# Optimization experiments

Measured on AMD Instinct MI355X. Metric: run time of the kernel, lower is better.

## Reference

```python
import jax, jax.numpy as jnp
import numpy as np

TY = 10  # decoder loop uses the global Ty=10 in the original code


def _bi_lstm_dir(X, Wih, Whh, b, n_hidden):
    # X: (m, T, F); returns hidden states (m, T, n_hidden). Gate order: i,f,g,o.
    m = X.shape[0]
    def step(carry, x_t):
        h, c = carry
        g = x_t @ Wih.T + h @ Whh.T + b
        i, f, gg, o = jnp.split(g, 4, axis=-1)
        c = jax.nn.sigmoid(f) * c + jax.nn.sigmoid(i) * jnp.tanh(gg)
        h = jax.nn.sigmoid(o) * jnp.tanh(c)
        return (h, c), h
    h0 = jnp.zeros((m, n_hidden), X.dtype)
    _, hs = jax.lax.scan(step, (h0, h0), jnp.swapaxes(X, 0, 1))
    return jnp.swapaxes(hs, 0, 1)


def setup_inputs() -> dict:
    key = jax.random.key(0)
    ks = jax.random.split(key, 17)
    m, Tx, F = 256, 256, 128
    n_a, n_s, vocab, attn_h = 256, 512, 1024, 10
    def w(k, shape, fan_in):
        return (jax.random.normal(k, shape, jnp.float32) / np.sqrt(fan_in)).astype(jnp.float32)
    return {
        "X": jax.random.normal(ks[0], (m, Tx, F), jnp.float32),
        "Wih_f": w(ks[1], (4 * n_a, F), F),
        "Whh_f": w(ks[2], (4 * n_a, n_a), n_a),
        "b_f": w(ks[3], (4 * n_a,), n_a),
        "Wih_b": w(ks[4], (4 * n_a, F), F),
        "Whh_b": w(ks[5], (4 * n_a, n_a), n_a),
        "b_b": w(ks[6], (4 * n_a,), n_a),
        "W1": w(ks[7], (attn_h, 2 * n_a + n_s), 2 * n_a + n_s),
        "b1": w(ks[8], (attn_h,), attn_h),
        "W2": w(ks[9], (1, attn_h), attn_h),
        "b2": w(ks[10], (1,), attn_h),
        "Wc_ih": w(ks[11], (4 * n_s, n_s), n_s),
        "Wc_hh": w(ks[12], (4 * n_s, n_s), n_s),
        "bc": w(ks[13], (4 * n_s,), n_s),
        "Wfc": w(ks[14], (vocab, n_s), n_s),
        "bfc": w(ks[15], (vocab,), n_s),
    }


def reference(X, Wih_f, Whh_f, b_f, Wih_b, Whh_b, b_b, W1, b1, W2, b2, Wc_ih, Wc_hh, bc, Wfc, bfc):
    m, Tx, _ = X.shape
    n_a = Whh_f.shape[1]
    n_s = Wc_hh.shape[1]
    # bidirectional encoder
    a_f = _bi_lstm_dir(X, Wih_f, Whh_f, b_f, n_a)
    a_b = _bi_lstm_dir(X[:, ::-1], Wih_b, Whh_b, b_b, n_a)[:, ::-1]
    a = jnp.concatenate([a_f, a_b], axis=-1)  # (m, Tx, 2*n_a)
    # decoder: initial h_n = zeros(m, 2, n_a).flatten(1) == zeros(m, n_s) since n_s = 2*n_a
    s = jnp.zeros((m, n_s), X.dtype)
    c = jnp.zeros((m, n_s), X.dtype)
    outs = []
    for _ in range(TY):
        sp = jnp.broadcast_to(s[:, None, :], (m, Tx, n_s))
        concat = jnp.concatenate([a, sp], axis=-1)           # (m, Tx, 2*n_a + n_s)
        e = jnp.tanh(concat @ W1.T + b1)                     # (m, Tx, 10)
        scores = jax.nn.relu(e @ W2.T + b2)                  # (m, Tx, 1)
        alphas = jax.nn.softmax(scores, axis=1)              # softmax over Tx
        context = jnp.sum(alphas * a, axis=1)                # (m, 2*n_a) == (m, n_s)
        g = context @ Wc_ih.T + s @ Wc_hh.T + bc             # LSTMCell
        i, f, gg, o = jnp.split(g, 4, axis=-1)
        c = jax.nn.sigmoid(f) * c + jax.nn.sigmoid(i) * jnp.tanh(gg)
        s = jax.nn.sigmoid(o) * jnp.tanh(c)
        outs.append(s @ Wfc.T + bfc)                         # (m, vocab)
    return jnp.stack(outs, axis=1)                           # (m, Ty, vocab)
```

## Files before the change

kernel.cpp:

```cpp
#include <hip/hip_runtime.h>
#include <hip/hip_bf16.h>
#include <hip/hip_cooperative_groups.h>

namespace cg = cooperative_groups;

#define TXN 256
#define NA 256
#define NF 128
#define NS 512
#define TYN 10
#define VOCAB 1024

#define A_STR 392
#define W_STR 392
#define WL_OFF (64 * W_STR)
#define AH_OFF (2 * 64 * W_STR)
#define AL_OFF (AH_OFF + 32 * A_STR)
#define PRE_OFF_US (AL_OFF + 32 * A_STR)
#define ENC_LDS_BYTES (150528 + 32 * 68 * 4 + 64 * 4)

#define D_STR 264
#define D_WH 0
#define D_WL (64 * D_STR)
#define D_AH (2 * 64 * D_STR)
#define D_AL (D_AH + 32 * D_STR)
#define D_PRE_US (D_AL + 32 * D_STR)
#define DEC_LDS_BYTES (101376 + 32 * 68 * 4 + 64 * 4)

typedef __attribute__((ext_vector_type(8))) short bf16x8;
typedef __attribute__((ext_vector_type(4))) float f32x4;

__device__ __forceinline__ float fsigmoid(float x) { return 1.f / (1.f + __expf(-x)); }
__device__ __forceinline__ float ftanh(float x)    { return 1.f - 2.f / (1.f + __expf(2.f * x)); }

__device__ __forceinline__ void split_bf16(float v, unsigned short& hi, unsigned short& lo) {
    __hip_bfloat16 h = __float2bfloat16(v);
    float rem = v - __bfloat162float(h);
    __hip_bfloat16 l = __float2bfloat16(rem);
    hi = *reinterpret_cast<unsigned short*>(&h);
    lo = *reinterpret_cast<unsigned short*>(&l);
}

__global__ __launch_bounds__(256, 1) void encoder_kernel(
    const float* __restrict__ X,
    const float* __restrict__ Wih_f, const float* __restrict__ Whh_f, const float* __restrict__ b_f,
    const float* __restrict__ Wih_b, const float* __restrict__ Whh_b, const float* __restrict__ b_b,
    float* __restrict__ a, unsigned int* __restrict__ bar)
{
    extern __shared__ unsigned char smem_raw[];
    unsigned short* Wh  = (unsigned short*)smem_raw;
    unsigned short* Wl  = (unsigned short*)smem_raw + WL_OFF;
    unsigned short* Ahh = (unsigned short*)smem_raw + AH_OFF;
    unsigned short* All = (unsigned short*)smem_raw + AL_OFF;
    float* Pre = (float*)(smem_raw + (size_t)PRE_OFF_US * 2);
    float* bsh = Pre + 32 * 68;

    const int tid = threadIdx.x;
    const int dir = blockIdx.x & 1;
    const int bid = blockIdx.x >> 1;
    const int i0 = (bid >> 4) * 32;
    const int j0 = (bid & 15) * 16;
    const int grp = dir * 8 + (bid >> 4);
    const int myjb = bid & 15;
    unsigned int* slots = bar + grp * 16;

    const float* __restrict__ Wih = dir ? Wih_b : Wih_f;
    const float* __restrict__ Whh = dir ? Whh_b : Whh_f;
    const float* __restrict__ bv  = dir ? b_b  : b_f;

    const int jl = tid & 15;
    const int ip = tid >> 4;
    const int iA = ip * 2;

    if (tid < 64) bsh[tid] = bv[(tid >> 4) * NA + j0 + (tid & 15)];
    for (int r = 0; r < 64; ++r) {
        int row = (r >> 4) * NA + j0 + (r & 15);
        unsigned short hi, lo;
        split_bf16(Whh[(size_t)row * NA + tid], hi, lo);
        Wh[r * W_STR + tid] = hi;
        Wl[r * W_STR + tid] = lo;
        if (tid < NF) {
            split_bf16(Wih[(size_t)row * NF + tid], hi, lo);
            Wh[r * W_STR + 256 + tid] = hi;
            Wl[r * W_STR + 256 + tid] = lo;
        }
    }

    #pragma unroll 4
    for (int r = 0; r < 32; ++r) {
        Ahh[r * A_STR + tid] = 0;
        All[r * A_STR + tid] = 0;
    }
    {
        const int t0 = dir ? (TXN - 1) : 0;
        const int kx = tid & 127;
        const int rbase = tid >> 7;
        #pragma unroll 4
        for (int rr = 0; rr < 16; ++rr) {
            int r = rr * 2 + rbase;
            float v = X[((size_t)(i0 + r) * TXN + t0) * NF + kx];
            unsigned short hi, lo;
            split_bf16(v, hi, lo);
            Ahh[r * A_STR + 256 + kx] = hi;
            All[r * A_STR + 256 + kx] = lo;
        }
    }

    float c0 = 0.f, c1 = 0.f;

    const int lane = tid & 63;
    const int wv   = tid >> 6;
    const int rt   = wv >> 1;
    const int g0   = (wv & 1) * 2;
    const int ln   = lane & 15;
    const int quad = lane >> 4;
    const unsigned short* pAh = Ahh + (rt * 16 + ln) * A_STR + quad * 8;
    const unsigned short* pAl = All + (rt * 16 + ln) * A_STR + quad * 8;
    const unsigned short* pW0h = Wh + (g0 * 16 + ln) * W_STR + quad * 8;
    const unsigned short* pW0l = Wl + (g0 * 16 + ln) * W_STR + quad * 8;
    const unsigned short* pW1h = pW0h + 16 * W_STR;
    const unsigned short* pW1l = pW0l + 16 * W_STR;

    for (int step = 0; step < TXN; ++step) {
        const int t = dir ? (TXN - 1 - step) : step;

        if (step != 0) {
            const int tprev = dir ? (t + 1) : (t - 1);
            const int jb = tid >> 4;
            while (__hip_atomic_load(&slots[jb], __ATOMIC_RELAXED,
                                     __HIP_MEMORY_SCOPE_AGENT) < (unsigned)step) {}
            float hv[32];
            #pragma unroll
            for (int r = 0; r < 32; ++r) {
                hv[r] = __hip_atomic_load(
                    &a[(((size_t)(i0 + r) * TXN + tprev) << 9) + dir * NA + tid],
                    __ATOMIC_RELAXED, __HIP_MEMORY_SCOPE_AGENT);
            }
            #pragma unroll
            for (int r = 0; r < 32; ++r) {
                unsigned short hi, lo;
                split_bf16(hv[r], hi, lo);
                Ahh[r * A_STR + tid] = hi;
                All[r * A_STR + tid] = lo;
            }
        }
        __syncthreads();

        f32x4 a0e = {0.f,0.f,0.f,0.f}, a0o = {0.f,0.f,0.f,0.f};
        f32x4 a1e = {0.f,0.f,0.f,0.f}, a1o = {0.f,0.f,0.f,0.f};
        #pragma unroll
        for (int kp = 0; kp < 6; ++kp) {
            {
                const int kc = kp * 2;
                bf16x8 fah = *(const bf16x8*)(pAh + kc * 32);
                bf16x8 fal = *(const bf16x8*)(pAl + kc * 32);
                bf16x8 w0h = *(const bf16x8*)(pW0h + kc * 32);
                bf16x8 w0l = *(const bf16x8*)(pW0l + kc * 32);
                bf16x8 w1h = *(const bf16x8*)(pW1h + kc * 32);
                bf16x8 w1l = *(const bf16x8*)(pW1l + kc * 32);
                a0e = __builtin_amdgcn_mfma_f32_16x16x32_bf16(fal, w0h, a0e, 0, 0, 0);
                a0e = __builtin_amdgcn_mfma_f32_16x16x32_bf16(fah, w0l, a0e, 0, 0, 0);
                a0e = __builtin_amdgcn_mfma_f32_16x16x32_bf16(fah, w0h, a0e, 0, 0, 0);
                a1e = __builtin_amdgcn_mfma_f32_16x16x32_bf16(fal, w1h, a1e, 0, 0, 0);
                a1e = __builtin_amdgcn_mfma_f32_16x16x32_bf16(fah, w1l, a1e, 0, 0, 0);
                a1e = __builtin_amdgcn_mfma_f32_16x16x32_bf16(fah, w1h, a1e, 0, 0, 0);
            }
            {
                const int kc = kp * 2 + 1;
                bf16x8 fah = *(const bf16x8*)(pAh + kc * 32);
                bf16x8 fal = *(const bf16x8*)(pAl + kc * 32);
                bf16x8 w0h = *(const bf16x8*)(pW0h + kc * 32);
                bf16x8 w0l = *(const bf16x8*)(pW0l + kc * 32);
                bf16x8 w1h = *(const bf16x8*)(pW1h + kc * 32);
                bf16x8 w1l = *(const bf16x8*)(pW1l + kc * 32);
                a0o = __builtin_amdgcn_mfma_f32_16x16x32_bf16(fal, w0h, a0o, 0, 0, 0);
                a0o = __builtin_amdgcn_mfma_f32_16x16x32_bf16(fah, w0l, a0o, 0, 0, 0);
                a0o = __builtin_amdgcn_mfma_f32_16x16x32_bf16(fah, w0h, a0o, 0, 0, 0);
                a1o = __builtin_amdgcn_mfma_f32_16x16x32_bf16(fal, w1h, a1o, 0, 0, 0);
                a1o = __builtin_amdgcn_mfma_f32_16x16x32_bf16(fah, w1l, a1o, 0, 0, 0);
                a1o = __builtin_amdgcn_mfma_f32_16x16x32_bf16(fah, w1h, a1o, 0, 0, 0);
            }
        }
        #pragma unroll
        for (int reg = 0; reg < 4; ++reg) {
            int prow = rt * 16 + quad * 4 + reg;
            Pre[prow * 68 + g0 * 16 + ln]       = a0e[reg] + a0o[reg];
            Pre[prow * 68 + (g0 + 1) * 16 + ln] = a1e[reg] + a1o[reg];
        }
        __syncthreads();

        float h0, h1;
        {
            float gi = fsigmoid(Pre[iA * 68 +      jl] + bsh[jl]);
            float gf = fsigmoid(Pre[iA * 68 + 16 + jl] + bsh[16 + jl]);
            float gg = ftanh  (Pre[iA * 68 + 32 + jl] + bsh[32 + jl]);
            float go = fsigmoid(Pre[iA * 68 + 48 + jl] + bsh[48 + jl]);
            c0 = gf * c0 + gi * gg;
            h0 = go * ftanh(c0);
        }
        {
            float gi = fsigmoid(Pre[(iA + 1) * 68 +      jl] + bsh[jl]);
            float gf = fsigmoid(Pre[(iA + 1) * 68 + 16 + jl] + bsh[16 + jl]);
            float gg = ftanh  (Pre[(iA + 1) * 68 + 32 + jl] + bsh[32 + jl]);
            float go = fsigmoid(Pre[(iA + 1) * 68 + 48 + jl] + bsh[48 + jl]);
            c1 = gf * c1 + gi * gg;
            h1 = go * ftanh(c1);
        }
        __hip_atomic_store(
            &a[(((size_t)(i0 + iA)     * TXN + t) << 9) + dir * NA + j0 + jl],
            h0, __ATOMIC_RELAXED, __HIP_MEMORY_SCOPE_AGENT);
        __hip_atomic_store(
            &a[(((size_t)(i0 + iA + 1) * TXN + t) << 9) + dir * NA + j0 + jl],
            h1, __ATOMIC_RELAXED, __HIP_MEMORY_SCOPE_AGENT);

        if (step != TXN - 1) {
            __syncthreads();
            if (tid == 0) {
                __hip_atomic_store(&slots[myjb], (unsigned)(step + 1),
                                   __ATOMIC_RELAXED, __HIP_MEMORY_SCOPE_AGENT);
            }
            {
                const int tn = dir ? (t - 1) : (t + 1);
                const int kx = tid & 127;
                const int rbase = tid >> 7;
                #pragma unroll 4
                for (int rr = 0; rr < 16; ++rr) {
                    int r = rr * 2 + rbase;
                    float v = X[((size_t)(i0 + r) * TXN + tn) * NF + kx];
                    unsigned short hi, lo;
                    split_bf16(v, hi, lo);
                    Ahh[r * A_STR + 256 + kx] = hi;
                    All[r * A_STR + 256 + kx] = lo;
                }
            }
        }
    }
}

__global__ __launch_bounds__(256) void wsplit_cat(
    const float* __restrict__ Wc_ih, const float* __restrict__ Wc_hh,
    unsigned short* __restrict__ Wh, unsigned short* __restrict__ Wl)
{
    int idx = blockIdx.x * 256 + threadIdx.x;
    int r = idx >> 10, k = idx & 1023;
    float v = (k < 512) ? Wc_ih[(size_t)r * 512 + k] : Wc_hh[(size_t)r * 512 + (k - 512)];
    unsigned short hi, lo;
    split_bf16(v, hi, lo);
    Wh[idx] = hi; Wl[idx] = lo;
}

__global__ __launch_bounds__(256) void wsplit_fc(
    const float* __restrict__ Wfc,
    unsigned short* __restrict__ Wh, unsigned short* __restrict__ Wl)
{
    int idx = blockIdx.x * 256 + threadIdx.x;
    unsigned short hi, lo;
    split_bf16(Wfc[idx], hi, lo);
    Wh[idx] = hi; Wl[idx] = lo;
}

__global__ __launch_bounds__(256, 1) void gates_kernel(
    const float* __restrict__ xcat,
    const unsigned short* __restrict__ Wch,
    const unsigned short* __restrict__ Wcl,
    const float* __restrict__ bc,
    float* __restrict__ c_buf,
    float* __restrict__ s_buf,
    float* __restrict__ xc_out)
{
    extern __shared__ unsigned char smem_raw[];
    unsigned short* Wh = (unsigned short*)smem_raw + D_WH;
    unsigned short* Wl = (unsigned short*)smem_raw + D_WL;
    unsigned short* Ah = (unsigned short*)smem_raw + D_AH;
    unsigned short* Al = (unsigned short*)smem_raw + D_AL;
    float* Pre = (float*)(smem_raw + (size_t)D_PRE_US * 2);
    float* bsh = Pre + 32 * 68;

    const int tid = threadIdx.x;
    const int i0 = blockIdx.x * 32;
    const int j0 = blockIdx.y * 16;

    if (tid < 64) bsh[tid] = bc[(tid >> 4) * 512 + j0 + (tid & 15)];

    const int lane = tid & 63;
    const int wv   = tid >> 6;
    const int rt   = wv >> 1;
    const int g0   = (wv & 1) * 2;
    const int ln   = lane & 15;
    const int quad = lane >> 4;
    const unsigned short* pAh = Ah + (rt * 16 + ln) * D_STR + quad * 8;
    const unsigned short* pAl = Al + (rt * 16 + ln) * D_STR + quad * 8;
    const unsigned short* pW0h = Wh + (g0 * 16 + ln) * D_STR + quad * 8;
    const unsigned short* pW0l = Wl + (g0 * 16 + ln) * D_STR + quad * 8;
    const unsigned short* pW1h = pW0h + 16 * D_STR;
    const unsigned short* pW1l = pW0l + 16 * D_STR;

    const int rW = tid >> 2;
    const int qW = (tid & 3) * 64;
    const int rowg = (rW >> 4) * 512 + j0 + (rW & 15);

    f32x4 a0 = {0.f,0.f,0.f,0.f}, a1 = {0.f,0.f,0.f,0.f};

    for (int ch = 0; ch < 4; ++ch) {
        const int kc0 = ch * 256;
        __syncthreads();
        #pragma unroll 8
        for (int r = 0; r < 32; ++r) {
            float v = xcat[(size_t)(i0 + r) * 1024 + kc0 + tid];
            unsigned short hi, lo;
            split_bf16(v, hi, lo);
            Ah[r * D_STR + tid] = hi;
            Al[r * D_STR + tid] = lo;
        }
        {
            const size_t base = (size_t)rowg * 1024 + kc0 + qW;
            #pragma unroll
            for (int i = 0; i < 8; ++i) {
                *(bf16x8*)&Wh[rW * D_STR + qW + i * 8] = *(const bf16x8*)&Wch[base + i * 8];
                *(bf16x8*)&Wl[rW * D_STR + qW + i * 8] = *(const bf16x8*)&Wcl[base + i * 8];
            }
        }
        __syncthreads();
        #pragma unroll
        for (int kc = 0; kc < 8; ++kc) {
            bf16x8 fah = *(const bf16x8*)(pAh + kc * 32);
            bf16x8 fal = *(const bf16x8*)(pAl + kc * 32);
            bf16x8 w0h = *(const bf16x8*)(pW0h + kc * 32);
            bf16x8 w0l = *(const bf16x8*)(pW0l + kc * 32);
            bf16x8 w1h = *(const bf16x8*)(pW1h + kc * 32);
            bf16x8 w1l = *(const bf16x8*)(pW1l + kc * 32);
            a0 = __builtin_amdgcn_mfma_f32_16x16x32_bf16(fal, w0h, a0, 0, 0, 0);
            a0 = __builtin_amdgcn_mfma_f32_16x16x32_bf16(fah, w0l, a0, 0, 0, 0);
            a0 = __builtin_amdgcn_mfma_f32_16x16x32_bf16(fah, w0h, a0, 0, 0, 0);
            a1 = __builtin_amdgcn_mfma_f32_16x16x32_bf16(fal, w1h, a1, 0, 0, 0);
            a1 = __builtin_amdgcn_mfma_f32_16x16x32_bf16(fah, w1l, a1, 0, 0, 0);
            a1 = __builtin_amdgcn_mfma_f32_16x16x32_bf16(fah, w1h, a1, 0, 0, 0);
        }
    }
    #pragma unroll
    for (int reg = 0; reg < 4; ++reg) {
        int prow = rt * 16 + quad * 4 + reg;
        Pre[prow * 68 + g0 * 16 + ln]       = a0[reg];
        Pre[prow * 68 + (g0 + 1) * 16 + ln] = a1[reg];
    }
    __syncthreads();

    const int jl = tid & 15;
    const int iA = (tid >> 4) * 2;
    #pragma unroll
    for (int rr = 0; rr < 2; ++rr) {
        int r = iA + rr;
        float gi = fsigmoid(Pre[r * 68 +      jl] + bsh[jl]);
        float gf = fsigmoid(Pre[r * 68 + 16 + jl] + bsh[16 + jl]);
        float gg = ftanh  (Pre[r * 68 + 32 + jl] + bsh[32 + jl]);
        float go = fsigmoid(Pre[r * 68 + 48 + jl] + bsh[48 + jl]);
        size_t ci = (size_t)(i0 + r) * 512 + j0 + jl;
        float cn = gf * c_buf[ci] + gi * gg;
        c_buf[ci] = cn;
        float h = go * ftanh(cn);
        s_buf[ci] = h;
        xc_out[(size_t)(i0 + r) * 1024 + 512 + j0 + jl] = h;
    }
}

__global__ __launch_bounds__(256, 1) void logits_kernel(
    const float* __restrict__ s_buf,
    const unsigned short* __restrict__ Wfh,
    const unsigned short* __restrict__ Wfl,
    const float* __restrict__ bfc,
    float* __restrict__ out, int ty)
{
    extern __shared__ unsigned char smem_raw[];
    unsigned short* Wh = (unsigned short*)smem_raw + D_WH;
    unsigned short* Wl = (unsigned short*)smem_raw + D_WL;
    unsigned short* Ah = (unsigned short*)smem_raw + D_AH;
    unsigned short* Al = (unsigned short*)smem_raw + D_AL;

    const int tid = threadIdx.x;
    const int i0 = blockIdx.x * 32;
    const int v0 = blockIdx.y * 64;

    const int lane = tid & 63;
    const int wv   = tid >> 6;
    const int rt   = wv >> 1;
    const int ct   = wv & 1;
    const int ln   = lane & 15;
    const int quad = lane >> 4;
    const unsigned short* pAh = Ah + (rt * 16 + ln) * D_STR + quad * 8;
    const unsigned short* pAl = Al + (rt * 16 + ln) * D_STR + quad * 8;
    const unsigned short* pW0h = Wh + (ct * 32 + ln) * D_STR + quad * 8;
    const unsigned short* pW0l = Wl + (ct * 32 + ln) * D_STR + quad * 8;
    const unsigned short* pW1h = pW0h + 16 * D_STR;
    const unsigned short* pW1l = pW0l + 16 * D_STR;

    const int rW = tid >> 2;
    const int qW = (tid & 3) * 64;

    f32x4 a0 = {0.f,0.f,0.f,0.f}, a1 = {0.f,0.f,0.f,0.f};

    for (int ch = 0; ch < 2; ++ch) {
        const int kc0 = ch * 256;
        __syncthreads();
        #pragma unroll 8
        for (int r = 0; r < 32; ++r) {
            float v = s_buf[(size_t)(i0 + r) * 512 + kc0 + tid];
            unsigned short hi, lo;
            split_bf16(v, hi, lo);
            Ah[r * D_STR + tid] = hi;
            Al[r * D_STR + tid] = lo;
        }
        {
            const size_t base = (size_t)(v0 + rW) * 512 + kc0 + qW;
            #pragma unroll
            for (int i = 0; i < 8; ++i) {
                *(bf16x8*)&Wh[rW * D_STR + qW + i * 8] = *(const bf16x8*)&Wfh[base + i * 8];
                *(bf16x8*)&Wl[rW * D_STR + qW + i * 8] = *(const bf16x8*)&Wfl[base + i * 8];
            }
        }
        __syncthreads();
        #pragma unroll
        for (int kc = 0; kc < 8; ++kc) {
            bf16x8 fah = *(const bf16x8*)(pAh + kc * 32);
            bf16x8 fal = *(const bf16x8*)(pAl + kc * 32);
            bf16x8 w0h = *(const bf16x8*)(pW0h + kc * 32);
            bf16x8 w0l = *(const bf16x8*)(pW0l + kc * 32);
            bf16x8 w1h = *(const bf16x8*)(pW1h + kc * 32);
            bf16x8 w1l = *(const bf16x8*)(pW1l + kc * 32);
            a0 = __builtin_amdgcn_mfma_f32_16x16x32_bf16(fal, w0h, a0, 0, 0, 0);
            a0 = __builtin_amdgcn_mfma_f32_16x16x32_bf16(fah, w0l, a0, 0, 0, 0);
            a0 = __builtin_amdgcn_mfma_f32_16x16x32_bf16(fah, w0h, a0, 0, 0, 0);
            a1 = __builtin_amdgcn_mfma_f32_16x16x32_bf16(fal, w1h, a1, 0, 0, 0);
            a1 = __builtin_amdgcn_mfma_f32_16x16x32_bf16(fah, w1l, a1, 0, 0, 0);
            a1 = __builtin_amdgcn_mfma_f32_16x16x32_bf16(fah, w1h, a1, 0, 0, 0);
        }
    }
    #pragma unroll
    for (int reg = 0; reg < 4; ++reg) {
        int row = i0 + rt * 16 + quad * 4 + reg;
        int col0 = v0 + ct * 32 + ln;
        out[(size_t)row * (TYN * VOCAB) + ty * VOCAB + col0]      = a0[reg] + bfc[col0];
        out[(size_t)row * (TYN * VOCAB) + ty * VOCAB + col0 + 16] = a1[reg] + bfc[col0 + 16];
    }
}

__global__ __launch_bounds__(256) void attn_prep(
    const float* __restrict__ a, const float* __restrict__ W1,
    const float* __restrict__ b1, float* __restrict__ aW1)
{
    __shared__ float Wsh[10][516];
    __shared__ float red[64][10][4];
    const int tid = threadIdx.x;
    for (int idx = tid; idx < 10 * 512; idx += 256) {
        int o = idx >> 9, k = idx & 511;
        Wsh[o][k] = W1[o * 1024 + k];
    }
    __syncthreads();
    const int r = tid >> 2, kq = tid & 3;
    const float* ar = a + ((size_t)blockIdx.x * 64 + r) * 512 + kq * 128;
    float acc[10] = {};
    for (int k = 0; k < 128; k += 4) {
        float4 v = *(const float4*)&ar[k];
        #pragma unroll
        for (int o = 0; o < 10; ++o) {
            float4 w = *(const float4*)&Wsh[o][kq * 128 + k];
            acc[o] += v.x * w.x + v.y * w.y + v.z * w.z + v.w * w.w;
        }
    }
    #pragma unroll
    for (int o = 0; o < 10; ++o) red[r][o][kq] = acc[o];
    __syncthreads();
    for (int idx = tid; idx < 640; idx += 256) {
        int rr = idx / 10, o = idx % 10;
        float s = red[rr][o][0] + red[rr][o][1] + red[rr][o][2] + red[rr][o][3] + b1[o];
        aW1[((size_t)blockIdx.x * 64 + rr) * 10 + o] = s;
    }
}

__global__ __launch_bounds__(256) void attn_kernel(
    const float* __restrict__ aW1,
    const float* __restrict__ s_buf,
    const float* __restrict__ W1,
    const float* __restrict__ W2,
    const float* __restrict__ b2,
    const float* __restrict__ a,
    float* __restrict__ xcat)
{
    __shared__ float sh_s[10];
    __shared__ float sh_w2[10];
    __shared__ float sred[160];
    __shared__ float red[256];
    __shared__ float al[256];
    __shared__ float4 ctxred[256];
    const int i = blockIdx.x;
    const int tid = threadIdx.x;

    if (tid < 160) {
        int o = tid >> 4, part = tid & 15;
        const float* srow = s_buf + (size_t)i * 512;
        const float* wrow = W1 + o * 1024 + 512;
        float p = 0.f;
        for (int k = part; k < 512; k += 16) p += srow[k] * wrow[k];
        sred[tid] = p;
    }
    __syncthreads();
    if (tid < 10) {
        float v = 0.f;
        #pragma unroll
        for (int p = 0; p < 16; ++p) v += sred[tid * 16 + p];
        sh_s[tid] = v;
        sh_w2[tid] = W2[tid];
    }
    __syncthreads();

    float sum = b2[0];
    const float* ar = aW1 + ((size_t)i * TXN + tid) * 10;
    #pragma unroll
    for (int h = 0; h < 10; ++h) {
        float e = ftanh(ar[h] + sh_s[h]);
        sum += e * sh_w2[h];
    }
    float sc = fmaxf(sum, 0.f);

    red[tid] = sc;
    __syncthreads();
    for (int s = 128; s > 0; s >>= 1) {
        if (tid < s) red[tid] = fmaxf(red[tid], red[tid + s]);
        __syncthreads();
    }
    float mx = red[0];
    __syncthreads();
    float p = __expf(sc - mx);
    red[tid] = p;
    __syncthreads();
    for (int s = 128; s > 0; s >>= 1) {
        if (tid < s) red[tid] += red[tid + s];
        __syncthreads();
    }
    float inv = 1.f / red[0];
    al[tid] = p * inv;
    __syncthreads();

    const int half = tid >> 7;
    const int q    = tid & 127;
    const float* abase = a + (size_t)i * TXN * NS + q * 4;
    float4 acc = make_float4(0.f, 0.f, 0.f, 0.f);
    #pragma unroll 8
    for (int t = half; t < TXN; t += 2) {
        float w = al[t];
        float4 v = *(const float4*)&abase[(size_t)t * NS];
        acc.x += w * v.x; acc.y += w * v.y; acc.z += w * v.z; acc.w += w * v.w;
    }
    ctxred[tid] = acc;
    __syncthreads();
    if (tid < 128) {
        float4 e = ctxred[tid];
        float4 o = ctxred[tid + 128];
        float4 r4 = make_float4(e.x + o.x, e.y + o.y, e.z + o.z, e.w + o.w);
        *(float4*)&xcat[(size_t)i * 1024 + tid * 4] = r4;
    }
}

extern "C" void kernel_launch(void* const* d_in, const int* in_sizes, int n_in,
                              void* d_out, int out_size, void* d_ws, size_t ws_size,
                              hipStream_t stream)
{
    const float* X     = (const float*)d_in[0];
    const float* Wih_f = (const float*)d_in[1];
    const float* Whh_f = (const float*)d_in[2];
    const float* b_f   = (const float*)d_in[3];
    const float* Wih_b = (const float*)d_in[4];
    const float* Whh_b = (const float*)d_in[5];
    const float* b_b   = (const float*)d_in[6];
    const float* W1    = (const float*)d_in[7];
    const float* b1    = (const float*)d_in[8];
    const float* W2    = (const float*)d_in[9];
    const float* b2    = (const float*)d_in[10];
    const float* Wc_ih = (const float*)d_in[11];
    const float* Wc_hh = (const float*)d_in[12];
    const float* bc    = (const float*)d_in[13];
    const float* Wfc   = (const float*)d_in[14];
    const float* bfc   = (const float*)d_in[15];
    float* out = (float*)d_out;
    float* ws  = (float*)d_ws;

    float* c_buf = ws;
    float* s_buf = ws + 131072;
    float* xcat  = ws + 262144;
    float* a     = ws + 524288;
    float* aW1   = ws + 34078720;
    unsigned short* Wch = (unsigned short*)(ws + 34734080);
    unsigned short* Wcl = (unsigned short*)(ws + 35782656);
    unsigned short* Wfh = (unsigned short*)(ws + 36831232);
    unsigned short* Wfl = (unsigned short*)(ws + 37093376);
    unsigned int* bar = (unsigned int*)(ws + 37358080);

    static int attrs_set = 0;
    if (!attrs_set) {
        hipFuncSetAttribute(reinterpret_cast<const void*>(encoder_kernel),
                            hipFuncAttributeMaxDynamicSharedMemorySize, ENC_LDS_BYTES);
        hipFuncSetAttribute(reinterpret_cast<const void*>(gates_kernel),
                            hipFuncAttributeMaxDynamicSharedMemorySize, DEC_LDS_BYTES);
        hipFuncSetAttribute(reinterpret_cast<const void*>(logits_kernel),
                            hipFuncAttributeMaxDynamicSharedMemorySize, DEC_LDS_BYTES);
        attrs_set = 1;
    }

    hipMemsetAsync(c_buf, 0, (size_t)524288 * sizeof(float), stream);
    hipMemsetAsync(bar, 0, 16 * 16 * sizeof(unsigned int), stream);

    wsplit_cat<<<8192, 256, 0, stream>>>(Wc_ih, Wc_hh, Wch, Wcl);
    wsplit_fc<<<2048, 256, 0, stream>>>(Wfc, Wfh, Wfl);

    {
        void* args[] = { (void*)&X, (void*)&Wih_f, (void*)&Whh_f, (void*)&b_f,
                         (void*)&Wih_b, (void*)&Whh_b, (void*)&b_b, (void*)&a, (void*)&bar };
        hipLaunchCooperativeKernel(reinterpret_cast<void*>(encoder_kernel),
                                   dim3(256), dim3(256), args, ENC_LDS_BYTES, stream);
    }

    attn_prep<<<1024, 256, 0, stream>>>(a, W1, b1, aW1);

    for (int ty = 0; ty < TYN; ++ty) {
        attn_kernel<<<256, 256, 0, stream>>>(aW1, s_buf, W1, W2, b2, a, xcat);
        gates_kernel<<<dim3(8, 32), 256, DEC_LDS_BYTES, stream>>>(
            xcat, Wch, Wcl, bc, c_buf, s_buf, xcat);
        logits_kernel<<<dim3(8, 16), 256, DEC_LDS_BYTES, stream>>>(
            s_buf, Wfh, Wfl, bfc, out, ty);
    }
}
```

Baseline: 2.194 ms.

## Fuse decoder attention, gates and logits into one persistent cooperative kernel

The 30 per-step decoder launches (attention, LSTM gates, logits for each of 10 output steps) are replaced by a single persistent cooperative kernel of 256 blocks. The blocks coordinate through per-tile flag slots in global memory, with agent-scope atomic loads and stores. The cell state now stays in registers, and the hidden state is double-buffered across two buffers. This removes launch overhead and the round trips through global memory between steps. In exchange it adds spin-wait synchronisation across blocks and a dependency on all 256 blocks being co-resident.

```diff
diff --git a/kernel.cpp b/kernel.cpp
--- a/kernel.cpp
+++ b/kernel.cpp
@@ -39,6 +39,19 @@
     __hip_bfloat16 l = __float2bfloat16(rem);
     hi = *reinterpret_cast<unsigned short*>(&h);
     lo = *reinterpret_cast<unsigned short*>(&l);
+}
+
+__device__ __forceinline__ float agent_ld(const float* p) {
+    return __hip_atomic_load(p, __ATOMIC_RELAXED, __HIP_MEMORY_SCOPE_AGENT);
+}
+__device__ __forceinline__ void agent_st(float* p, float v) {
+    __hip_atomic_store(p, v, __ATOMIC_RELAXED, __HIP_MEMORY_SCOPE_AGENT);
+}
+__device__ __forceinline__ unsigned flag_ld(const unsigned* p) {
+    return __hip_atomic_load(p, __ATOMIC_RELAXED, __HIP_MEMORY_SCOPE_AGENT);
+}
+__device__ __forceinline__ void flag_st(unsigned* p, unsigned v) {
+    __hip_atomic_store(p, v, __ATOMIC_RELAXED, __HIP_MEMORY_SCOPE_AGENT);
 }
 
 __global__ __launch_bounds__(256, 1) void encoder_kernel(
@@ -127,14 +140,11 @@
         if (step != 0) {
             const int tprev = dir ? (t + 1) : (t - 1);
             const int jb = tid >> 4;
-            while (__hip_atomic_load(&slots[jb], __ATOMIC_RELAXED,
-                                     __HIP_MEMORY_SCOPE_AGENT) < (unsigned)step) {}
+            while (flag_ld(&slots[jb]) < (unsigned)step) {}
             float hv[32];
             #pragma unroll
             for (int r = 0; r < 32; ++r) {
-                hv[r] = __hip_atomic_load(
-                    &a[(((size_t)(i0 + r) * TXN + tprev) << 9) + dir * NA + tid],
-                    __ATOMIC_RELAXED, __HIP_MEMORY_SCOPE_AGENT);
+                hv[r] = agent_ld(&a[(((size_t)(i0 + r) * TXN + tprev) << 9) + dir * NA + tid]);
             }
             #pragma unroll
             for (int r = 0; r < 32; ++r) {
@@ -206,19 +216,12 @@
             c1 = gf * c1 + gi * gg;
             h1 = go * ftanh(c1);
         }
-        __hip_atomic_store(
-            &a[(((size_t)(i0 + iA)     * TXN + t) << 9) + dir * NA + j0 + jl],
-            h0, __ATOMIC_RELAXED, __HIP_MEMORY_SCOPE_AGENT);
-        __hip_atomic_store(
-            &a[(((size_t)(i0 + iA + 1) * TXN + t) << 9) + dir * NA + j0 + jl],
-            h1, __ATOMIC_RELAXED, __HIP_MEMORY_SCOPE_AGENT);
+        agent_st(&a[(((size_t)(i0 + iA)     * TXN + t) << 9) + dir * NA + j0 + jl], h0);
+        agent_st(&a[(((size_t)(i0 + iA + 1) * TXN + t) << 9) + dir * NA + j0 + jl], h1);
 
         if (step != TXN - 1) {
             __syncthreads();
-            if (tid == 0) {
-                __hip_atomic_store(&slots[myjb], (unsigned)(step + 1),
-                                   __ATOMIC_RELAXED, __HIP_MEMORY_SCOPE_AGENT);
-            }
+            if (tid == 0) flag_st(&slots[myjb], (unsigned)(step + 1));
             {
                 const int tn = dir ? (t - 1) : (t + 1);
                 const int kx = tid & 127;
@@ -259,190 +262,6 @@
     Wh[idx] = hi; Wl[idx] = lo;
 }
 
-__global__ __launch_bounds__(256, 1) void gates_kernel(
-    const float* __restrict__ xcat,
-    const unsigned short* __restrict__ Wch,
-    const unsigned short* __restrict__ Wcl,
-    const float* __restrict__ bc,
-    float* __restrict__ c_buf,
-    float* __restrict__ s_buf,
-    float* __restrict__ xc_out)
-{
-    extern __shared__ unsigned char smem_raw[];
-    unsigned short* Wh = (unsigned short*)smem_raw + D_WH;
-    unsigned short* Wl = (unsigned short*)smem_raw + D_WL;
-    unsigned short* Ah = (unsigned short*)smem_raw + D_AH;
-    unsigned short* Al = (unsigned short*)smem_raw + D_AL;
-    float* Pre = (float*)(smem_raw + (size_t)D_PRE_US * 2);
-    float* bsh = Pre + 32 * 68;
-
-    const int tid = threadIdx.x;
-    const int i0 = blockIdx.x * 32;
-    const int j0 = blockIdx.y * 16;
-
-    if (tid < 64) bsh[tid] = bc[(tid >> 4) * 512 + j0 + (tid & 15)];
-
-    const int lane = tid & 63;
-    const int wv   = tid >> 6;
-    const int rt   = wv >> 1;
-    const int g0   = (wv & 1) * 2;
-    const int ln   = lane & 15;
-    const int quad = lane >> 4;
-    const unsigned short* pAh = Ah + (rt * 16 + ln) * D_STR + quad * 8;
-    const unsigned short* pAl = Al + (rt * 16 + ln) * D_STR + quad * 8;
-    const unsigned short* pW0h = Wh + (g0 * 16 + ln) * D_STR + quad * 8;
-    const unsigned short* pW0l = Wl + (g0 * 16 + ln) * D_STR + quad * 8;
-    const unsigned short* pW1h = pW0h + 16 * D_STR;
-    const unsigned short* pW1l = pW0l + 16 * D_STR;
-
-    const int rW = tid >> 2;
-    const int qW = (tid & 3) * 64;
-    const int rowg = (rW >> 4) * 512 + j0 + (rW & 15);
-
-    f32x4 a0 = {0.f,0.f,0.f,0.f}, a1 = {0.f,0.f,0.f,0.f};
-
-    for (int ch = 0; ch < 4; ++ch) {
-        const int kc0 = ch * 256;
-        __syncthreads();
-        #pragma unroll 8
-        for (int r = 0; r < 32; ++r) {
-            float v = xcat[(size_t)(i0 + r) * 1024 + kc0 + tid];
-            unsigned short hi, lo;
-            split_bf16(v, hi, lo);
-            Ah[r * D_STR + tid] = hi;
-            Al[r * D_STR + tid] = lo;
-        }
-        {
-            const size_t base = (size_t)rowg * 1024 + kc0 + qW;
-            #pragma unroll
-            for (int i = 0; i < 8; ++i) {
-                *(bf16x8*)&Wh[rW * D_STR + qW + i * 8] = *(const bf16x8*)&Wch[base + i * 8];
-                *(bf16x8*)&Wl[rW * D_STR + qW + i * 8] = *(const bf16x8*)&Wcl[base + i * 8];
-            }
-        }
-        __syncthreads();
-        #pragma unroll
-        for (int kc = 0; kc < 8; ++kc) {
-            bf16x8 fah = *(const bf16x8*)(pAh + kc * 32);
-            bf16x8 fal = *(const bf16x8*)(pAl + kc * 32);
-            bf16x8 w0h = *(const bf16x8*)(pW0h + kc * 32);
-            bf16x8 w0l = *(const bf16x8*)(pW0l + kc * 32);
-            bf16x8 w1h = *(const bf16x8*)(pW1h + kc * 32);
-            bf16x8 w1l = *(const bf16x8*)(pW1l + kc * 32);
-            a0 = __builtin_amdgcn_mfma_f32_16x16x32_bf16(fal, w0h, a0, 0, 0, 0);
-            a0 = __builtin_amdgcn_mfma_f32_16x16x32_bf16(fah, w0l, a0, 0, 0, 0);
-            a0 = __builtin_amdgcn_mfma_f32_16x16x32_bf16(fah, w0h, a0, 0, 0, 0);
-            a1 = __builtin_amdgcn_mfma_f32_16x16x32_bf16(fal, w1h, a1, 0, 0, 0);
-            a1 = __builtin_amdgcn_mfma_f32_16x16x32_bf16(fah, w1l, a1, 0, 0, 0);
-            a1 = __builtin_amdgcn_mfma_f32_16x16x32_bf16(fah, w1h, a1, 0, 0, 0);
-        }
-    }
-    #pragma unroll
-    for (int reg = 0; reg < 4; ++reg) {
-        int prow = rt * 16 + quad * 4 + reg;
-        Pre[prow * 68 + g0 * 16 + ln]       = a0[reg];
-        Pre[prow * 68 + (g0 + 1) * 16 + ln] = a1[reg];
-    }
-    __syncthreads();
-
-    const int jl = tid & 15;
-    const int iA = (tid >> 4) * 2;
-    #pragma unroll
-    for (int rr = 0; rr < 2; ++rr) {
-        int r = iA + rr;
-        float gi = fsigmoid(Pre[r * 68 +      jl] + bsh[jl]);
-        float gf = fsigmoid(Pre[r * 68 + 16 + jl] + bsh[16 + jl]);
-        float gg = ftanh  (Pre[r * 68 + 32 + jl] + bsh[32 + jl]);
-        float go = fsigmoid(Pre[r * 68 + 48 + jl] + bsh[48 + jl]);
-        size_t ci = (size_t)(i0 + r) * 512 + j0 + jl;
-        float cn = gf * c_buf[ci] + gi * gg;
-        c_buf[ci] = cn;
-        float h = go * ftanh(cn);
-        s_buf[ci] = h;
-        xc_out[(size_t)(i0 + r) * 1024 + 512 + j0 + jl] = h;
-    }
-}
-
-__global__ __launch_bounds__(256, 1) void logits_kernel(
-    const float* __restrict__ s_buf,
-    const unsigned short* __restrict__ Wfh,
-    const unsigned short* __restrict__ Wfl,
-    const float* __restrict__ bfc,
-    float* __restrict__ out, int ty)
-{
-    extern __shared__ unsigned char smem_raw[];
-    unsigned short* Wh = (unsigned short*)smem_raw + D_WH;
-    unsigned short* Wl = (unsigned short*)smem_raw + D_WL;
-    unsigned short* Ah = (unsigned short*)smem_raw + D_AH;
-    unsigned short* Al = (unsigned short*)smem_raw + D_AL;
-
-    const int tid = threadIdx.x;
-    const int i0 = blockIdx.x * 32;
-    const int v0 = blockIdx.y * 64;
-
-    const int lane = tid & 63;
-    const int wv   = tid >> 6;
-    const int rt   = wv >> 1;
-    const int ct   = wv & 1;
-    const int ln   = lane & 15;
-    const int quad = lane >> 4;
-    const unsigned short* pAh = Ah + (rt * 16 + ln) * D_STR + quad * 8;
-    const unsigned short* pAl = Al + (rt * 16 + ln) * D_STR + quad * 8;
-    const unsigned short* pW0h = Wh + (ct * 32 + ln) * D_STR + quad * 8;
-    const unsigned short* pW0l = Wl + (ct * 32 + ln) * D_STR + quad * 8;
-    const unsigned short* pW1h = pW0h + 16 * D_STR;
-    const unsigned short* pW1l = pW0l + 16 * D_STR;
-
-    const int rW = tid >> 2;
-    const int qW = (tid & 3) * 64;
-
-    f32x4 a0 = {0.f,0.f,0.f,0.f}, a1 = {0.f,0.f,0.f,0.f};
-
-    for (int ch = 0; ch < 2; ++ch) {
-        const int kc0 = ch * 256;
-        __syncthreads();
-        #pragma unroll 8
-        for (int r = 0; r < 32; ++r) {
-            float v = s_buf[(size_t)(i0 + r) * 512 + kc0 + tid];
-            unsigned short hi, lo;
-            split_bf16(v, hi, lo);
-            Ah[r * D_STR + tid] = hi;
-            Al[r * D_STR + tid] = lo;
-        }
-        {
-            const size_t base = (size_t)(v0 + rW) * 512 + kc0 + qW;
-            #pragma unroll
-            for (int i = 0; i < 8; ++i) {
-                *(bf16x8*)&Wh[rW * D_STR + qW + i * 8] = *(const bf16x8*)&Wfh[base + i * 8];
-                *(bf16x8*)&Wl[rW * D_STR + qW + i * 8] = *(const bf16x8*)&Wfl[base + i * 8];
-            }
-        }
-        __syncthreads();
-        #pragma unroll
-        for (int kc = 0; kc < 8; ++kc) {
-            bf16x8 fah = *(const bf16x8*)(pAh + kc * 32);
-            bf16x8 fal = *(const bf16x8*)(pAl + kc * 32);
-            bf16x8 w0h = *(const bf16x8*)(pW0h + kc * 32);
-            bf16x8 w0l = *(const bf16x8*)(pW0l + kc * 32);
-            bf16x8 w1h = *(const bf16x8*)(pW1h + kc * 32);
-            bf16x8 w1l = *(const bf16x8*)(pW1l + kc * 32);
-            a0 = __builtin_amdgcn_mfma_f32_16x16x32_bf16(fal, w0h, a0, 0, 0, 0);
-            a0 = __builtin_amdgcn_mfma_f32_16x16x32_bf16(fah, w0l, a0, 0, 0, 0);
-            a0 = __builtin_amdgcn_mfma_f32_16x16x32_bf16(fah, w0h, a0, 0, 0, 0);
-            a1 = __builtin_amdgcn_mfma_f32_16x16x32_bf16(fal, w1h, a1, 0, 0, 0);
-            a1 = __builtin_amdgcn_mfma_f32_16x16x32_bf16(fah, w1l, a1, 0, 0, 0);
-            a1 = __builtin_amdgcn_mfma_f32_16x16x32_bf16(fah, w1h, a1, 0, 0, 0);
-        }
-    }
-    #pragma unroll
-    for (int reg = 0; reg < 4; ++reg) {
-        int row = i0 + rt * 16 + quad * 4 + reg;
-        int col0 = v0 + ct * 32 + ln;
-        out[(size_t)row * (TYN * VOCAB) + ty * VOCAB + col0]      = a0[reg] + bfc[col0];
-        out[(size_t)row * (TYN * VOCAB) + ty * VOCAB + col0 + 16] = a1[reg] + bfc[col0 + 16];
-    }
-}
-
 __global__ __launch_bounds__(256) void attn_prep(
     const float* __restrict__ a, const float* __restrict__ W1,
     const float* __restrict__ b1, float* __restrict__ aW1)
@@ -476,87 +295,284 @@
     }
 }
 
-__global__ __launch_bounds__(256) void attn_kernel(
+__global__ __launch_bounds__(256, 1) void decoder_kernel(
     const float* __restrict__ aW1,
-    const float* __restrict__ s_buf,
+    const float* __restrict__ a,
     const float* __restrict__ W1,
     const float* __restrict__ W2,
     const float* __restrict__ b2,
-    const float* __restrict__ a,
-    float* __restrict__ xcat)
+    const unsigned short* __restrict__ Wch,
+    const unsigned short* __restrict__ Wcl,
+    const float* __restrict__ bc,
+    const unsigned short* __restrict__ Wfh,
+    const unsigned short* __restrict__ Wfl,
+    const float* __restrict__ bfc,
+    float* __restrict__ sbufA,
+    float* __restrict__ sbufB,
+    float* __restrict__ xcat,
+    float* __restrict__ out,
+    unsigned int* __restrict__ slots)
 {
-    __shared__ float sh_s[10];
-    __shared__ float sh_w2[10];
-    __shared__ float sred[160];
-    __shared__ float red[256];
-    __shared__ float al[256];
-    __shared__ float4 ctxred[256];
-    const int i = blockIdx.x;
+    extern __shared__ unsigned char smem_raw[];
+    unsigned short* Wh = (unsigned short*)smem_raw + D_WH;
+    unsigned short* Wl = (unsigned short*)smem_raw + D_WL;
+    unsigned short* Ah = (unsigned short*)smem_raw + D_AH;
+    unsigned short* Al = (unsigned short*)smem_raw + D_AL;
+    float* Pre = (float*)(smem_raw + (size_t)D_PRE_US * 2);
+    float* F     = (float*)smem_raw;
+    float* Aal   = F;
+    float* Ared  = F + 256;
+    float* Asred = F + 512;
+    float* Ash_s = F + 672;
+    float* Ash_w2= F + 682;
+    float4* Actx = (float4*)(F + 704);
+
+    unsigned int* attn_slot  = slots;
+    unsigned int* gates_slot = slots + 256;
+    unsigned int* log_slot   = slots + 512;
+
     const int tid = threadIdx.x;
-
-    if (tid < 160) {
-        int o = tid >> 4, part = tid & 15;
-        const float* srow = s_buf + (size_t)i * 512;
-        const float* wrow = W1 + o * 1024 + 512;
-        float p = 0.f;
-        for (int k = part; k < 512; k += 16) p += srow[k] * wrow[k];
-        sred[tid] = p;
-    }
-    __syncthreads();
-    if (tid < 10) {
-        float v = 0.f;
+    const int b   = blockIdx.x;
+    const int it  = b >> 5;
+    const int jt  = b & 31;
+    const int i0  = it * 32;
+    const int j0  = jt * 16;
+    const int v0  = jt * 32;
+
+    const int lane = tid & 63;
+    const int wv   = tid >> 6;
+    const int rt   = wv >> 1;
+    const int g0   = (wv & 1) * 2;
+    const int ct   = wv & 1;
+    const int ln   = lane & 15;
+    const int quad = lane >> 4;
+    const int jl   = tid & 15;
+    const int iA   = (tid >> 4) * 2;
+
+    const unsigned short* pAh = Ah + (rt * 16 + ln) * D_STR + quad * 8;
+    const unsigned short* pAl = Al + (rt * 16 + ln) * D_STR + quad * 8;
+    const unsigned short* pGW0h = Wh + (g0 * 16 + ln) * D_STR + quad * 8;
+    const unsigned short* pGW0l = Wl + (g0 * 16 + ln) * D_STR + quad * 8;
+    const unsigned short* pGW1h = pGW0h + 16 * D_STR;
+    const unsigned short* pGW1l = pGW0l + 16 * D_STR;
+    const unsigned short* pLWh = Wh + (ct * 16 + ln) * D_STR + quad * 8;
+    const unsigned short* pLWl = Wl + (ct * 16 + ln) * D_STR + quad * 8;
+
+    const float bgi = bc[0 * 512 + j0 + jl];
+    const float bgf = bc[1 * 512 + j0 + jl];
+    const float bgg = bc[2 * 512 + j0 + jl];
+    const float bgo = bc[3 * 512 + j0 + jl];
+
+    float c0 = 0.f, c1 = 0.f;
+
+    for (int ty = 0; ty < TYN; ++ty) {
+        float* sp = (ty & 1) ? sbufB : sbufA;
+        float* sn = (ty & 1) ? sbufA : sbufB;
+
+        if (tid < 32) {
+            while (flag_ld(&gates_slot[it * 32 + tid]) < (unsigned)ty) {}
+        }
+        __syncthreads();
+
+        if (tid < 160) {
+            int o = tid >> 4, part = tid & 15;
+            const float* srow = sp + (size_t)b * 512;
+            const float* wrow = W1 + o * 1024 + 512;
+            float p = 0.f;
+            for (int k = part; k < 512; k += 16) p += agent_ld(&srow[k]) * wrow[k];
+            Asred[tid] = p;
+        }
+        __syncthreads();
+        if (tid < 10) {
+            float v = 0.f;
+            #pragma unroll
+            for (int p = 0; p < 16; ++p) v += Asred[tid * 16 + p];
+            Ash_s[tid] = v;
+            Ash_w2[tid] = W2[tid];
+        }
+        __syncthreads();
+
+        float sum = b2[0];
+        {
+            const float* ar = aW1 + ((size_t)b * TXN + tid) * 10;
+            #pragma unroll
+            for (int h = 0; h < 10; ++h) sum += ftanh(ar[h] + Ash_s[h]) * Ash_w2[h];
+        }
+        float sc = fmaxf(sum, 0.f);
+
+        Ared[tid] = sc;
+        __syncthreads();
+        for (int s = 128; s > 0; s >>= 1) {
+            if (tid < s) Ared[tid] = fmaxf(Ared[tid], Ared[tid + s]);
+            __syncthreads();
+        }
+        float mx = Ared[0];
+        __syncthreads();
+        float p = __expf(sc - mx);
+        Ared[tid] = p;
+        __syncthreads();
+        for (int s = 128; s > 0; s >>= 1) {
+            if (tid < s) Ared[tid] += Ared[tid + s];
+            __syncthreads();
+        }
+        float inv = 1.f / Ared[0];
+        Aal[tid] = p * inv;
+        __syncthreads();
+
+        {
+            const int half = tid >> 7;
+            const int q    = tid & 127;
+            const float* abase = a + (size_t)b * TXN * NS + q * 4;
+            float4 acc = make_float4(0.f, 0.f, 0.f, 0.f);
+            #pragma unroll 8
+            for (int t = half; t < TXN; t += 2) {
+                float w = Aal[t];
+                float4 v = *(const float4*)&abase[(size_t)t * NS];
+                acc.x += w * v.x; acc.y += w * v.y; acc.z += w * v.z; acc.w += w * v.w;
+            }
+            Actx[tid] = acc;
+        }
+        __syncthreads();
+        if (tid < 128) {
+            float4 e = Actx[tid];
+            float4 o = Actx[tid + 128];
+            float* dst = &xcat[(size_t)b * 512 + tid * 4];
+            agent_st(dst + 0, e.x + o.x);
+            agent_st(dst + 1, e.y + o.y);
+            agent_st(dst + 2, e.z + o.z);
+            agent_st(dst + 3, e.w + o.w);
+        }
+        __syncthreads();
+        if (tid == 0) flag_st(&attn_slot[b], (unsigned)(ty + 1));
+
+        if (tid < 32) {
+            while (flag_ld(&attn_slot[i0 + tid]) < (unsigned)(ty + 1)) {}
+        } else if (tid < 64) {
+            while (flag_ld(&gates_slot[it * 32 + (tid - 32)]) < (unsigned)ty) {}
+        } else if (tid < 96) {
+            while (flag_ld(&log_slot[it * 32 + (tid - 64)]) < (unsigned)ty) {}
+        }
+
+        f32x4 ga0 = {0.f,0.f,0.f,0.f}, ga1 = {0.f,0.f,0.f,0.f};
+        {
+            const int rW = tid >> 2;
+            const int qW = (tid & 3) * 64;
+            const int rowg = (rW >> 4) * 512 + j0 + (rW & 15);
+            for (int ch = 0; ch < 4; ++ch) {
+                const int kc0 = ch * 256;
+                __syncthreads();
+                #pragma unroll 8
+                for (int r = 0; r < 32; ++r) {
+                    float v;
+                    if (ch < 2) v = agent_ld(&xcat[(size_t)(i0 + r) * 512 + kc0 + tid]);
+                    else        v = agent_ld(&sp[(size_t)(i0 + r) * 512 + (kc0 - 512) + tid]);
+                    unsigned short hi, lo;
+                    split_bf16(v, hi, lo);
+                    Ah[r * D_STR + tid] = hi;
+                    Al[r * D_STR + tid] = lo;
+                }
+                {
+                    const size_t base = (size_t)rowg * 1024 + kc0 + qW;
+                    #pragma unroll
+                    for (int i = 0; i < 8; ++i) {
+                        *(bf16x8*)&Wh[rW * D_STR + qW + i * 8] = *(const bf16x8*)&Wch[base + i * 8];
+                        *(bf16x8*)&Wl[rW * D_STR + qW + i * 8] = *(const bf16x8*)&Wcl[base + i * 8];
+                    }
+                }
+                __syncthreads();
+                #pragma unroll
+                for (int kc = 0; kc < 8; ++kc) {
+                    bf16x8 fah = *(const bf16x8*)(pAh + kc * 32);
+                    bf16x8 fal = *(const bf16x8*)(pAl + kc * 32);
+                    bf16x8 w0h = *(const bf16x8*)(pGW0h + kc * 32);
+                    bf16x8 w0l = *(const bf16x8*)(pGW0l + kc * 32);
+                    bf16x8 w1h = *(const bf16x8*)(pGW1h + kc * 32);
+                    bf16x8 w1l = *(const bf16x8*)(pGW1l + kc * 32);
+                    ga0 = __builtin_amdgcn_mfma_f32_16x16x32_bf16(fal, w0h, ga0, 0, 0, 0);
+                    ga0 = __builtin_amdgcn_mfma_f32_16x16x32_bf16(fah, w0l, ga0, 0, 0, 0);
+                    ga0 = __builtin_amdgcn_mfma_f32_16x16x32_bf16(fah, w0h, ga0, 0, 0, 0);
+                    ga1 = __builtin_amdgcn_mfma_f32_16x16x32_bf16(fal, w1h, ga1, 0, 0, 0);
+                    ga1 = __builtin_amdgcn_mfma_f32_16x16x32_bf16(fah, w1l, ga1, 0, 0, 0);
+                    ga1 = __builtin_amdgcn_mfma_f32_16x16x32_bf16(fah, w1h, ga1, 0, 0, 0);
+                }
+            }
+        }
+        __syncthreads();
         #pragma unroll
-        for (int p = 0; p < 16; ++p) v += sred[tid * 16 + p];
-        sh_s[tid] = v;
-        sh_w2[tid] = W2[tid];
-    }
-    __syncthreads();
-
-    float sum = b2[0];
-    const float* ar = aW1 + ((size_t)i * TXN + tid) * 10;
-    #pragma unroll
-    for (int h = 0; h < 10; ++h) {
-        float e = ftanh(ar[h] + sh_s[h]);
-        sum += e * sh_w2[h];
-    }
-    float sc = fmaxf(sum, 0.f);
-
-    red[tid] = sc;
-    __syncthreads();
-    for (int s = 128; s > 0; s >>= 1) {
-        if (tid < s) red[tid] = fmaxf(red[tid], red[tid + s]);
-        __syncthreads();
-    }
-    float mx = red[0];
-    __syncthreads();
-    float p = __expf(sc - mx);
-    red[tid] = p;
-    __syncthreads();
-    for (int s = 128; s > 0; s >>= 1) {
-        if (tid < s) red[tid] += red[tid + s];
-        __syncthreads();
-    }
-    float inv = 1.f / red[0];
-    al[tid] = p * inv;
-    __syncthreads();
-
-    const int half = tid >> 7;
-    const int q    = tid & 127;
-    const float* abase = a + (size_t)i * TXN * NS + q * 4;
-    float4 acc = make_float4(0.f, 0.f, 0.f, 0.f);
-    #pragma unroll 8
-    for (int t = half; t < TXN; t += 2) {
-        float w = al[t];
-        float4 v = *(const float4*)&abase[(size_t)t * NS];
-        acc.x += w * v.x; acc.y += w * v.y; acc.z += w * v.z; acc.w += w * v.w;
-    }
-    ctxred[tid] = acc;
-    __syncthreads();
-    if (tid < 128) {
-        float4 e = ctxred[tid];
-        float4 o = ctxred[tid + 128];
-        float4 r4 = make_float4(e.x + o.x, e.y + o.y, e.z + o.z, e.w + o.w);
-        *(float4*)&xcat[(size_t)i * 1024 + tid * 4] = r4;
+        for (int reg = 0; reg < 4; ++reg) {
+            int prow = rt * 16 + quad * 4 + reg;
+            Pre[prow * 68 + g0 * 16 + ln]       = ga0[reg];
+            Pre[prow * 68 + (g0 + 1) * 16 + ln] = ga1[reg];
+        }
+        __syncthreads();
+
+        {
+            float gi = fsigmoid(Pre[iA * 68 +      jl] + bgi);
+            float gf = fsigmoid(Pre[iA * 68 + 16 + jl] + bgf);
+            float gg = ftanh  (Pre[iA * 68 + 32 + jl] + bgg);
+            float go = fsigmoid(Pre[iA * 68 + 48 + jl] + bgo);
+            c0 = gf * c0 + gi * gg;
+            agent_st(&sn[(size_t)(i0 + iA) * 512 + j0 + jl], go * ftanh(c0));
+        }
+        {
+            float gi = fsigmoid(Pre[(iA + 1) * 68 +      jl] + bgi);
+            float gf = fsigmoid(Pre[(iA + 1) * 68 + 16 + jl] + bgf);
+            float gg = ftanh  (Pre[(iA + 1) * 68 + 32 + jl] + bgg);
+            float go = fsigmoid(Pre[(iA + 1) * 68 + 48 + jl] + bgo);
+            c1 = gf * c1 + gi * gg;
+            agent_st(&sn[(size_t)(i0 + iA + 1) * 512 + j0 + jl], go * ftanh(c1));
+        }
+        __syncthreads();
+        if (tid == 0) flag_st(&gates_slot[it * 32 + jt], (unsigned)(ty + 1));
+
+        if (tid < 32) {
+            while (flag_ld(&gates_slot[it * 32 + tid]) < (unsigned)(ty + 1)) {}
+        }
+
+        f32x4 lacc = {0.f,0.f,0.f,0.f};
+        {
+            const int rW = tid >> 3;
+            const int qW = (tid & 7) * 32;
+            for (int ch = 0; ch < 2; ++ch) {
+                const int kc0 = ch * 256;
+                __syncthreads();
+                #pragma unroll 8
+                for (int r = 0; r < 32; ++r) {
+                    float v = agent_ld(&sn[(size_t)(i0 + r) * 512 + kc0 + tid]);
+                    unsigned short hi, lo;
+                    split_bf16(v, hi, lo);
+                    Ah[r * D_STR + tid] = hi;
+                    Al[r * D_STR + tid] = lo;
+                }
+                {
+                    const size_t base = (size_t)(v0 + rW) * 512 + kc0 + qW;
+                    #pragma unroll
+                    for (int i = 0; i < 4; ++i) {
+                        *(bf16x8*)&Wh[rW * D_STR + qW + i * 8] = *(const bf16x8*)&Wfh[base + i * 8];
+                        *(bf16x8*)&Wl[rW * D_STR + qW + i * 8] = *(const bf16x8*)&Wfl[base + i * 8];
+                    }
+                }
+                __syncthreads();
+                #pragma unroll
+                for (int kc = 0; kc < 8; ++kc) {
+                    bf16x8 fah = *(const bf16x8*)(pAh + kc * 32);
+                    bf16x8 fal = *(const bf16x8*)(pAl + kc * 32);
+                    bf16x8 wh  = *(const bf16x8*)(pLWh + kc * 32);
+                    bf16x8 wl  = *(const bf16x8*)(pLWl + kc * 32);
+                    lacc = __builtin_amdgcn_mfma_f32_16x16x32_bf16(fal, wh, lacc, 0, 0, 0);
+                    lacc = __builtin_amdgcn_mfma_f32_16x16x32_bf16(fah, wl, lacc, 0, 0, 0);
+                    lacc = __builtin_amdgcn_mfma_f32_16x16x32_bf16(fah, wh, lacc, 0, 0, 0);
+                }
+            }
+        }
+        #pragma unroll
+        for (int reg = 0; reg < 4; ++reg) {
+            int row = i0 + rt * 16 + quad * 4 + reg;
+            int col = v0 + ct * 16 + ln;
+            out[(size_t)row * (TYN * VOCAB) + ty * VOCAB + col] = lacc[reg] + bfc[col];
+        }
+        __syncthreads();
+        if (tid == 0) flag_st(&log_slot[it * 32 + jt], (unsigned)(ty + 1));
     }
 }
 
@@ -583,8 +599,8 @@
     float* out = (float*)d_out;
     float* ws  = (float*)d_ws;
 
-    float* c_buf = ws;
-    float* s_buf = ws + 131072;
+    float* sbufA = ws;
+    float* sbufB = ws + 131072;
     float* xcat  = ws + 262144;
     float* a     = ws + 524288;
     float* aW1   = ws + 34078720;
@@ -592,21 +608,20 @@
     unsigned short* Wcl = (unsigned short*)(ws + 35782656);
     unsigned short* Wfh = (unsigned short*)(ws + 36831232);
     unsigned short* Wfl = (unsigned short*)(ws + 37093376);
-    unsigned int* bar = (unsigned int*)(ws + 37358080);
+    unsigned int* dslots = (unsigned int*)(ws + 37355520);
+    unsigned int* bar    = (unsigned int*)(ws + 37356288);
 
     static int attrs_set = 0;
     if (!attrs_set) {
         hipFuncSetAttribute(reinterpret_cast<const void*>(encoder_kernel),
                             hipFuncAttributeMaxDynamicSharedMemorySize, ENC_LDS_BYTES);
-        hipFuncSetAttribute(reinterpret_cast<const void*>(gates_kernel),
-                            hipFuncAttributeMaxDynamicSharedMemorySize, DEC_LDS_BYTES);
-        hipFuncSetAttribute(reinterpret_cast<const void*>(logits_kernel),
+        hipFuncSetAttribute(reinterpret_cast<const void*>(decoder_kernel),
                             hipFuncAttributeMaxDynamicSharedMemorySize, DEC_LDS_BYTES);
         attrs_set = 1;
     }
 
-    hipMemsetAsync(c_buf, 0, (size_t)524288 * sizeof(float), stream);
-    hipMemsetAsync(bar, 0, 16 * 16 * sizeof(unsigned int), stream);
+    hipMemsetAsync(sbufA, 0, (size_t)131072 * sizeof(float), stream);
+    hipMemsetAsync(dslots, 0, (768 + 256) * sizeof(unsigned int), stream);
 
     wsplit_cat<<<8192, 256, 0, stream>>>(Wc_ih, Wc_hh, Wch, Wcl);
     wsplit_fc<<<2048, 256, 0, stream>>>(Wfc, Wfh, Wfl);
@@ -620,11 +635,13 @@
 
     attn_prep<<<1024, 256, 0, stream>>>(a, W1, b1, aW1);
 
-    for (int ty = 0; ty < TYN; ++ty) {
-        attn_kernel<<<256, 256, 0, stream>>>(aW1, s_buf, W1, W2, b2, a, xcat);
-        gates_kernel<<<dim3(8, 32), 256, DEC_LDS_BYTES, stream>>>(
-            xcat, Wch, Wcl, bc, c_buf, s_buf, xcat);
-        logits_kernel<<<dim3(8, 16), 256, DEC_LDS_BYTES, stream>>>(
-            s_buf, Wfh, Wfl, bfc, out, ty);
-    }
-}
+    {
+        void* args[] = { (void*)&aW1, (void*)&a, (void*)&W1, (void*)&W2, (void*)&b2,
+                         (void*)&Wch, (void*)&Wcl, (void*)&bc,
+                         (void*)&Wfh, (void*)&Wfl, (void*)&bfc,
+                         (void*)&sbufA, (void*)&sbufB, (void*)&xcat,
+                         (void*)&out, (void*)&dslots };
+        hipLaunchCooperativeKernel(reinterpret_cast<void*>(decoder_kernel),
+                                   dim3(256), dim3(256), args, DEC_LDS_BYTES, stream);
+    }
+}
```

After: 2.425 ms. 1.11x slower.
